# Performance work log

Hardware: AMD Instinct MI355X
Metric: run time of the kernel (lower is better)

The kernel has to match this reference:

```python
import jax, jax.numpy as jnp
import numpy as np

B, T, D, H, FF, L = 4, 2048, 512, 8, 2048, 4
IN_SIZE = 32
PAST, FUT = 128, 128
HD = D // H
EPS = 1e-5


def _layer_norm(x, g, b):
    m = jnp.mean(x, axis=-1, keepdims=True)
    v = jnp.mean((x - m) ** 2, axis=-1, keepdims=True)
    return (x - m) / jnp.sqrt(v + EPS) * g + b


def setup_inputs() -> dict:
    key = jax.random.key(0)
    ks = jax.random.split(key, 20)
    s = 0.02
    inp = {
        "beatmap_features": jax.random.normal(ks[0], (B, T, IN_SIZE), jnp.float32),
        "positions": jax.random.normal(ks[1], (B, T, 2), jnp.float32),
        "proj_w": jax.random.normal(ks[2], (D, IN_SIZE), jnp.float32) * s,
        "proj_b": jnp.zeros((D,), jnp.float32),
        "pos_enc": jax.random.normal(ks[3], (T, D), jnp.float32),
        # stacked per-layer params, leading dim L
        "qkv_w": jax.random.normal(ks[4], (L, 3 * D, D), jnp.float32) * s,
        "qkv_b": jnp.zeros((L, 3 * D), jnp.float32),
        "out_w": jax.random.normal(ks[5], (L, D, D), jnp.float32) * s,
        "out_b": jnp.zeros((L, D), jnp.float32),
        "ff1_w": jax.random.normal(ks[6], (L, FF, D), jnp.float32) * s,
        "ff1_b": jnp.zeros((L, FF), jnp.float32),
        "ff2_w": jax.random.normal(ks[7], (L, D, FF), jnp.float32) * s,
        "ff2_b": jnp.zeros((L, D), jnp.float32),
        "ln1_g": jnp.ones((L, D), jnp.float32),
        "ln1_b": jnp.zeros((L, D), jnp.float32),
        "ln2_g": jnp.ones((L, D), jnp.float32),
        "ln2_b": jnp.zeros((L, D), jnp.float32),
    }
    return inp


def reference(beatmap_features, positions, proj_w, proj_b, pos_enc,
              qkv_w, qkv_b, out_w, out_b, ff1_w, ff1_b, ff2_w, ff2_b,
              ln1_g, ln1_b, ln2_g, ln2_b):
    # positions only perturbed by noise during training; eval forward ignores it.
    x = beatmap_features @ proj_w.T + proj_b + pos_enc[None]  # [B,T,D]

    # banded local-window additive mask: allow j in [i-PAST, i+FUT]
    i = jnp.arange(T)[:, None]
    j = jnp.arange(T)[None, :]
    allow = (j >= i - PAST) & (j <= i + FUT)
    mask = jnp.where(allow, 0.0, -jnp.inf).astype(x.dtype)  # [T,T]

    scale = 1.0 / jnp.sqrt(jnp.asarray(HD, x.dtype))

    def enc_layer(x, p):
        qkvw, qkvb, ow, ob, f1w, f1b, f2w, f2b, g1, b1, g2, b2 = p
        qkv = x @ qkvw.T + qkvb                         # [B,T,3D]
        q, k, v = jnp.split(qkv, 3, axis=-1)
        q = q.reshape(B, T, H, HD).transpose(0, 2, 1, 3)  # [B,H,T,HD]
        k = k.reshape(B, T, H, HD).transpose(0, 2, 1, 3)
        v = v.reshape(B, T, H, HD).transpose(0, 2, 1, 3)
        scores = jnp.einsum('bhqd,bhkd->bhqk', q, k) * scale + mask
        attn = jax.nn.softmax(scores, axis=-1)
        o = jnp.einsum('bhqk,bhkd->bhqd', attn, v)
        o = o.transpose(0, 2, 1, 3).reshape(B, T, D) @ ow.T + ob
        x = _layer_norm(x + o, g1, b1)                  # post-norm (PyTorch default)
        h = jax.nn.relu(x @ f1w.T + f1b) @ f2w.T + f2b
        x = _layer_norm(x + h, g2, b2)
        return x, None

    params = (qkv_w, qkv_b, out_w, out_b, ff1_w, ff1_b, ff2_w, ff2_b,
              ln1_g, ln1_b, ln2_g, ln2_b)
    x, _ = jax.lax.scan(enc_layer, x, params)
    return x
```

## Files before the change

kernel.cpp:

```cpp
#include <hip/hip_runtime.h>
#include <hip/hip_bf16.h>

#define B_ 4
#define T_ 2048
#define D_ 512
#define H_ 8
#define FF_ 2048
#define L_ 4
#define NTOK 8192
#define EPS_ 1e-5f

typedef __hip_bfloat16 bf16;
typedef __attribute__((ext_vector_type(8))) short short8;
typedef __attribute__((ext_vector_type(4))) float floatx4;

__device__ __forceinline__ float bf2f(short s) {
    union { unsigned u; float f; } cv;
    cv.u = ((unsigned)(unsigned short)s) << 16;
    return cv.f;
}
__device__ __forceinline__ short f2bs(float f) {
    union { bf16 b; short s; } cv;
    cv.b = __float2bfloat16(f);
    return cv.s;
}

__global__ __launch_bounds__(256) void prep_kernel(
    const float* __restrict__ s0, const float* __restrict__ s1,
    const float* __restrict__ s2, const float* __restrict__ s3,
    bf16* __restrict__ dst, const float* __restrict__ pw, float* __restrict__ pwT)
{
    int bid = blockIdx.x;
    if (bid >= 12288) {
        int idx = (bid - 12288) * 256 + threadIdx.x;
        int d = idx >> 5, k = idx & 31;
        pwT[k * D_ + d] = pw[idx];
        return;
    }
    long i = (long)bid * 256 + threadIdx.x;
    const float* src; long off;
    if (i < 786432)       { src = s0; off = i; }
    else if (i < 1048576) { src = s1; off = i - 786432; }
    else if (i < 2097152) { src = s2; off = i - 1048576; }
    else                  { src = s3; off = i - 2097152; }
    float4 v = ((const float4*)src)[off];
    union { short s[4]; uint2 u; } pk;
    pk.s[0] = f2bs(v.x); pk.s[1] = f2bs(v.y);
    pk.s[2] = f2bs(v.z); pk.s[3] = f2bs(v.w);
    *(uint2*)((short*)dst + i * 4) = pk.u;
}

__global__ __launch_bounds__(256) void proj_kernel(
    const float* __restrict__ feat, const float* __restrict__ pwT,
    const float* __restrict__ pb, const float* __restrict__ pe,
    bf16* __restrict__ xb)
{
    __shared__ float fs[16][32];
    int tok0 = blockIdx.x * 16;
    int tid = threadIdx.x;
    {
        float2 v = ((const float2*)(feat + (size_t)tok0 * 32))[tid];
        fs[tid >> 4][(tid & 15) * 2]     = v.x;
        fs[tid >> 4][(tid & 15) * 2 + 1] = v.y;
    }
    int d0 = tid * 2;
    float w0[32], w1[32];
    #pragma unroll
    for (int k = 0; k < 32; k++) {
        float2 wv = *(const float2*)(pwT + k * D_ + d0);
        w0[k] = wv.x; w1[k] = wv.y;
    }
    float2 pbv = *(const float2*)(pb + d0);
    __syncthreads();
    #pragma unroll 4
    for (int tok = 0; tok < 16; tok++) {
        int t = (tok0 + tok) & (T_ - 1);
        float s0 = pbv.x, s1 = pbv.y;
        #pragma unroll
        for (int k = 0; k < 32; k++) {
            float f = fs[tok][k];
            s0 += f * w0[k]; s1 += f * w1[k];
        }
        float2 pev = *(const float2*)(pe + (size_t)t * D_ + d0);
        s0 += pev.x; s1 += pev.y;
        size_t o = (size_t)(tok0 + tok) * D_ + d0;
        union { struct { short a, b; } s; unsigned u; } pk;
        pk.s.a = f2bs(s0); pk.s.b = f2bs(s1);
        *(unsigned*)((short*)xb + o) = pk.u;
    }
}

template <int RELU>
__global__ __launch_bounds__(256) void gemm_bf16_kernel(
    const short* __restrict__ A, const short* __restrict__ W,
    const float* __restrict__ bias, bf16* __restrict__ Cb,
    int M, int N, int Kstride, int Kloc)
{
    __shared__ __align__(16) short lds[128 * 136];
    int bm = blockIdx.y * 128, bn = blockIdx.x * 128;
    int kbase = blockIdx.z * Kloc;
    int tid = threadIdx.x;
    int w = tid >> 6, lane = tid & 63;
    int wm = (w >> 1) * 64, wn = (w & 1) * 64;

    floatx4 acc[4][4];
    #pragma unroll
    for (int i = 0; i < 4; i++)
        #pragma unroll
        for (int j = 0; j < 4; j++)
            acc[i][j] = (floatx4){0.f, 0.f, 0.f, 0.f};

    int r0 = tid >> 2;
    int c0 = tid & 3;
    int slot = (c0 ^ ((r0 >> 1) & 3)) * 8;
    const short* Arow0 = A + (size_t)(bm + r0) * Kstride + kbase + c0 * 8;
    const short* Arow1 = A + (size_t)(bm + r0 + 64) * Kstride + kbase + c0 * 8;
    const short* Brow0 = W + (size_t)(bn + r0) * Kstride + kbase + c0 * 8;
    const short* Brow1 = W + (size_t)(bn + r0 + 64) * Kstride + kbase + c0 * 8;

    int lrow = lane & 15, lk = lane >> 4;

    short8 ea0, ea1, eb0, eb1;
    short8 oa0, oa1, ob0, ob1;
    ea0 = *(const short8*)(Arow0);       ea1 = *(const short8*)(Arow1);
    eb0 = *(const short8*)(Brow0);       eb1 = *(const short8*)(Brow1);
    oa0 = *(const short8*)(Arow0 + 32);  oa1 = *(const short8*)(Arow1 + 32);
    ob0 = *(const short8*)(Brow0 + 32);  ob1 = *(const short8*)(Brow1 + 32);

    int nIter = Kloc >> 5;
    for (int it = 0; it < nIter; it += 2) {
        #pragma unroll
        for (int half = 0; half < 2; half++) {
            short* As = lds + half * 8192;
            short* Bs = lds + half * 8192 + 4096;
            if (half == 0) {
                *(short8*)&As[r0 * 32 + slot] = ea0;
                *(short8*)&As[(r0 + 64) * 32 + slot] = ea1;
                *(short8*)&Bs[r0 * 32 + slot] = eb0;
                *(short8*)&Bs[(r0 + 64) * 32 + slot] = eb1;
            } else {
                *(short8*)&As[r0 * 32 + slot] = oa0;
                *(short8*)&As[(r0 + 64) * 32 + slot] = oa1;
                *(short8*)&Bs[r0 * 32 + slot] = ob0;
                *(short8*)&Bs[(r0 + 64) * 32 + slot] = ob1;
            }
            __syncthreads();
            int kn = (it + half + 2) * 32;
            if (kn < Kloc) {
                if (half == 0) {
                    ea0 = *(const short8*)(Arow0 + kn);
                    ea1 = *(const short8*)(Arow1 + kn);
                    eb0 = *(const short8*)(Brow0 + kn);
                    eb1 = *(const short8*)(Brow1 + kn);
                } else {
                    oa0 = *(const short8*)(Arow0 + kn);
                    oa1 = *(const short8*)(Arow1 + kn);
                    ob0 = *(const short8*)(Brow0 + kn);
                    ob1 = *(const short8*)(Brow1 + kn);
                }
            }
            short8 af[4], bfr[4];
            #pragma unroll
            for (int i = 0; i < 4; i++) {
                int rr = wm + i * 16 + lrow;
                af[i] = *(const short8*)&As[rr * 32 + ((lk ^ ((rr >> 1) & 3)) * 8)];
                int nn = wn + i * 16 + lrow;
                bfr[i] = *(const short8*)&Bs[nn * 32 + ((lk ^ ((nn >> 1) & 3)) * 8)];
            }
            #pragma unroll
            for (int i = 0; i < 4; i++)
                #pragma unroll
                for (int j = 0; j < 4; j++)
                    acc[i][j] = __builtin_amdgcn_mfma_f32_16x16x32_bf16(
                        af[i], bfr[j], acc[i][j], 0, 0, 0);
        }
    }

    __syncthreads();

    int cl = lane & 15, rq = lane >> 4;
    bool z0 = (blockIdx.z == 0);
    #pragma unroll
    for (int i = 0; i < 4; i++) {
        #pragma unroll
        for (int j = 0; j < 4; j++) {
            int col = wn + j * 16 + cl;
            float bv = z0 ? bias[bn + col] : 0.f;
            #pragma unroll
            for (int r = 0; r < 4; r++) {
                int row = wm + i * 16 + rq * 4 + r;
                float v = acc[i][j][r] + bv;
                if (RELU) v = fmaxf(v, 0.f);
                lds[row * 136 + col] = f2bs(v);
            }
        }
    }
    __syncthreads();

    bf16* Cz = Cb + (size_t)blockIdx.z * M * N;
    #pragma unroll
    for (int s = 0; s < 8; s++) {
        int idx = tid + 256 * s;
        int r = idx >> 4, c8 = (idx & 15) * 8;
        short8 v = *(const short8*)&lds[r * 136 + c8];
        *(short8*)((short*)Cz + (size_t)(bm + r) * N + bn + c8) = v;
    }
}

__global__ __launch_bounds__(256, 4) void attn_kernel(
    const short* __restrict__ qkv, bf16* __restrict__ out)
{
    __shared__ __align__(16) short Qs[64 * 72];
    __shared__ __align__(16) short Ks[64 * 72];
    __shared__ __align__(16) short Vt[64 * 72];
    __shared__ __align__(16) short Ps[64 * 72];

    int q0 = blockIdx.x * 64;
    int bh = blockIdx.y;
    int b = bh >> 3, h = bh & 7;
    int tid = threadIdx.x;
    int w = tid >> 6, lane = tid & 63;
    int col = lane & 15, quad = lane >> 4;

    const size_t base = (size_t)b * T_ * 3 * D_;
    const int roww = 3 * D_;
    const int qoff = h * 64, koff = D_ + h * 64, voff = 2 * D_ + h * 64;

    #pragma unroll
    for (int i = 0; i < 2; i++) {
        int idx = tid + 256 * i;
        int r = idx >> 3, c8 = (idx & 7) * 8;
        *(short8*)&Qs[r * 72 + c8] =
            *(const short8*)(qkv + base + (size_t)(q0 + r) * roww + qoff + c8);
    }

    float l_r[4] = {0.f, 0.f, 0.f, 0.f};
    floatx4 Oacc[4];
    #pragma unroll
    for (int j = 0; j < 4; j++) Oacc[j] = (floatx4){0.f, 0.f, 0.f, 0.f};

    int klo = max(0, q0 - 128), khi = min(T_, q0 + 192);
    const float scale = 0.125f;
    int qrow = q0 + w * 16 + quad * 4;

    for (int kt = klo; kt < khi; kt += 64) {
        __syncthreads();
        #pragma unroll
        for (int i = 0; i < 2; i++) {
            int idx = tid + 256 * i;
            int r = idx >> 3, c8 = (idx & 7) * 8;
            *(short8*)&Ks[r * 72 + c8] =
                *(const short8*)(qkv + base + (size_t)(kt + r) * roww + koff + c8);
            short8 v = *(const short8*)(qkv + base + (size_t)(kt + r) * roww + voff + c8);
            #pragma unroll
            for (int u = 0; u < 8; u++) Vt[(c8 + u) * 72 + r] = v[u];
        }
        __syncthreads();

        short8 aq0 = *(const short8*)&Qs[(w * 16 + col) * 72 + quad * 8];
        short8 aq1 = *(const short8*)&Qs[(w * 16 + col) * 72 + 32 + quad * 8];
        floatx4 Sacc[4];
        #pragma unroll
        for (int j = 0; j < 4; j++) {
            short8 bk0 = *(const short8*)&Ks[(j * 16 + col) * 72 + quad * 8];
            short8 bk1 = *(const short8*)&Ks[(j * 16 + col) * 72 + 32 + quad * 8];
            floatx4 s = (floatx4){0.f, 0.f, 0.f, 0.f};
            s = __builtin_amdgcn_mfma_f32_16x16x32_bf16(aq0, bk0, s, 0, 0, 0);
            s = __builtin_amdgcn_mfma_f32_16x16x32_bf16(aq1, bk1, s, 0, 0, 0);
            Sacc[j] = s;
        }

        float ps[4] = {0.f, 0.f, 0.f, 0.f};
        #pragma unroll
        for (int j = 0; j < 4; j++) {
            int key = kt + j * 16 + col;
            #pragma unroll
            for (int r = 0; r < 4; r++) {
                int dj = key - (qrow + r);
                float p = (dj < -128 || dj > 128) ? 0.f : __expf(Sacc[j][r] * scale);
                ps[r] += p;
                Ps[(w * 16 + quad * 4 + r) * 72 + j * 16 + col] = f2bs(p);
            }
        }
        #pragma unroll
        for (int off = 1; off < 16; off <<= 1)
            #pragma unroll
            for (int r = 0; r < 4; r++)
                ps[r] += __shfl_xor(ps[r], off);
        #pragma unroll
        for (int r = 0; r < 4; r++) l_r[r] += ps[r];

        __syncthreads();

        short8 ap0 = *(const short8*)&Ps[(w * 16 + col) * 72 + quad * 8];
        short8 ap1 = *(const short8*)&Ps[(w * 16 + col) * 72 + 32 + quad * 8];
        #pragma unroll
        for (int j = 0; j < 4; j++) {
            short8 bv0 = *(const short8*)&Vt[(j * 16 + col) * 72 + quad * 8];
            short8 bv1 = *(const short8*)&Vt[(j * 16 + col) * 72 + 32 + quad * 8];
            Oacc[j] = __builtin_amdgcn_mfma_f32_16x16x32_bf16(ap0, bv0, Oacc[j], 0, 0, 0);
            Oacc[j] = __builtin_amdgcn_mfma_f32_16x16x32_bf16(ap1, bv1, Oacc[j], 0, 0, 0);
        }
    }

    float invl[4];
    #pragma unroll
    for (int r = 0; r < 4; r++) invl[r] = 1.0f / l_r[r];
    #pragma unroll
    for (int j = 0; j < 4; j++)
        #pragma unroll
        for (int r = 0; r < 4; r++)
            out[(size_t)(b * T_ + qrow + r) * D_ + h * 64 + j * 16 + col] =
                __float2bfloat16(Oacc[j][r] * invl[r]);
}

__global__ __launch_bounds__(256) void add_ln_kernel(
    const short* __restrict__ xb, const short* __restrict__ d0,
    const short* __restrict__ d1,
    const float* __restrict__ g, const float* __restrict__ bta,
    bf16* __restrict__ outb, float* __restrict__ outf)
{
    int wave = threadIdx.x >> 6, lane = threadIdx.x & 63;
    int row = blockIdx.x * 4 + wave;
    int c0 = lane * 8;
    size_t o = (size_t)row * D_ + c0;
    short8 xv = *(const short8*)(xb + o);
    short8 a0 = *(const short8*)(d0 + o);
    short8 a1 = *(const short8*)(d1 + o);
    float v[8];
    float s = 0.f;
    #pragma unroll
    for (int i = 0; i < 8; i++) {
        v[i] = bf2f(xv[i]) + bf2f(a0[i]) + bf2f(a1[i]);
        s += v[i];
    }
    #pragma unroll
    for (int off = 32; off > 0; off >>= 1) s += __shfl_xor(s, off);
    float mean = s * (1.0f / D_);
    float var = 0.f;
    #pragma unroll
    for (int i = 0; i < 8; i++) { float c = v[i] - mean; var += c * c; }
    #pragma unroll
    for (int off = 32; off > 0; off >>= 1) var += __shfl_xor(var, off);
    float inv = rsqrtf(var * (1.0f / D_) + EPS_);
    float4 g0 = *(const float4*)(g + c0), g1 = *(const float4*)(g + c0 + 4);
    float4 b0 = *(const float4*)(bta + c0), b1 = *(const float4*)(bta + c0 + 4);
    float ov[8];
    ov[0] = (v[0] - mean) * inv * g0.x + b0.x;
    ov[1] = (v[1] - mean) * inv * g0.y + b0.y;
    ov[2] = (v[2] - mean) * inv * g0.z + b0.z;
    ov[3] = (v[3] - mean) * inv * g0.w + b0.w;
    ov[4] = (v[4] - mean) * inv * g1.x + b1.x;
    ov[5] = (v[5] - mean) * inv * g1.y + b1.y;
    ov[6] = (v[6] - mean) * inv * g1.z + b1.z;
    ov[7] = (v[7] - mean) * inv * g1.w + b1.w;
    short8 ob;
    #pragma unroll
    for (int i = 0; i < 8; i++) ob[i] = f2bs(ov[i]);
    *(short8*)((short*)outb + o) = ob;
    if (outf) {
        *(float4*)(outf + o) = make_float4(ov[0], ov[1], ov[2], ov[3]);
        *(float4*)(outf + o + 4) = make_float4(ov[4], ov[5], ov[6], ov[7]);
    }
}

extern "C" void kernel_launch(void* const* d_in, const int* in_sizes, int n_in,
                              void* d_out, int out_size, void* d_ws, size_t ws_size,
                              hipStream_t stream)
{
    const float* feat    = (const float*)d_in[0];
    const float* proj_w  = (const float*)d_in[2];
    const float* proj_b  = (const float*)d_in[3];
    const float* pos_enc = (const float*)d_in[4];
    const float* qkv_w   = (const float*)d_in[5];
    const float* qkv_b   = (const float*)d_in[6];
    const float* out_w   = (const float*)d_in[7];
    const float* out_b   = (const float*)d_in[8];
    const float* ff1_w   = (const float*)d_in[9];
    const float* ff1_b   = (const float*)d_in[10];
    const float* ff2_w   = (const float*)d_in[11];
    const float* ff2_b   = (const float*)d_in[12];
    const float* ln1_g   = (const float*)d_in[13];
    const float* ln1_b   = (const float*)d_in[14];
    const float* ln2_g   = (const float*)d_in[15];
    const float* ln2_b   = (const float*)d_in[16];

    char* p = (char*)d_ws;
    float* pwT  = (float*)p;  p += (size_t)32 * D_ * 4;
    bf16* xb    = (bf16*)p;   p += (size_t)NTOK * D_ * 2;
    bf16* dpar  = (bf16*)p;   p += (size_t)2 * NTOK * D_ * 2;
    bf16* qkvb  = (bf16*)p;   p += (size_t)NTOK * 3 * D_ * 2;
    bf16* hbuf  = (bf16*)p;   p += (size_t)NTOK * FF_ * 2;
    bf16* abuf  = (bf16*)p;   p += (size_t)NTOK * D_ * 2;
    bf16* wq    = (bf16*)p;   p += (size_t)L_ * 3 * D_ * D_ * 2;
    bf16* wo    = (bf16*)p;   p += (size_t)L_ * D_ * D_ * 2;
    bf16* w1    = (bf16*)p;   p += (size_t)L_ * FF_ * D_ * 2;
    bf16* w2    = (bf16*)p;   p += (size_t)L_ * D_ * FF_ * 2;
    float* outp = (float*)d_out;

    prep_kernel<<<12288 + 64, 256, 0, stream>>>(
        qkv_w, out_w, ff1_w, ff2_w, wq, proj_w, pwT);

    proj_kernel<<<NTOK / 16, 256, 0, stream>>>(feat, pwT, proj_b, pos_enc, xb);

    for (int l = 0; l < L_; l++) {
        gemm_bf16_kernel<0><<<dim3(3 * D_ / 128, NTOK / 128, 1), 256, 0, stream>>>(
            (const short*)xb, (const short*)(wq + (size_t)l * 3 * D_ * D_),
            qkv_b + (size_t)l * 3 * D_, qkvb, NTOK, 3 * D_, D_, D_);
        attn_kernel<<<dim3(T_ / 64, B_ * H_), 256, 0, stream>>>((const short*)qkvb, abuf);
        gemm_bf16_kernel<0><<<dim3(D_ / 128, NTOK / 128, 2), 256, 0, stream>>>(
            (const short*)abuf, (const short*)(wo + (size_t)l * D_ * D_),
            out_b + (size_t)l * D_, dpar, NTOK, D_, D_, D_ / 2);
        add_ln_kernel<<<NTOK / 4, 256, 0, stream>>>(
            (const short*)xb, (const short*)dpar, (const short*)(dpar + (size_t)NTOK * D_),
            ln1_g + (size_t)l * D_, ln1_b + (size_t)l * D_, xb, nullptr);
        gemm_bf16_kernel<1><<<dim3(FF_ / 128, NTOK / 128, 1), 256, 0, stream>>>(
            (const short*)xb, (const short*)(w1 + (size_t)l * FF_ * D_),
            ff1_b + (size_t)l * FF_, hbuf, NTOK, FF_, D_, D_);
        gemm_bf16_kernel<0><<<dim3(D_ / 128, NTOK / 128, 2), 256, 0, stream>>>(
            (const short*)hbuf, (const short*)(w2 + (size_t)l * D_ * FF_),
            ff2_b + (size_t)l * D_, dpar, NTOK, D_, FF_, FF_ / 2);
        float* dst = (l == L_ - 1) ? outp : nullptr;
        add_ln_kernel<<<NTOK / 4, 256, 0, stream>>>(
            (const short*)xb, (const short*)dpar, (const short*)(dpar + (size_t)NTOK * D_),
            ln2_g + (size_t)l * D_, ln2_b + (size_t)l * D_, xb, dst);
    }
}
```

Measured before the change: 660.0 us.

## Swizzle block IDs across XCDs and register-prefetch next K/V tile in attention

Adds an XCD-aware block-index swizzle to the GEMM and attention kernels so that neighbouring tiles, which share operands, land on the same XCD and its L2. In the attention kernel, the next K/V tile is loaded from global memory into registers while the current tile is being computed, hiding global load latency behind the MFMA work. This raises register pressure in a kernel launched with occupancy bound 4. The swizzle assumes the total block count is divisible by 8.

```diff
diff --git a/kernel.cpp b/kernel.cpp
--- a/kernel.cpp
+++ b/kernel.cpp
@@ -23,6 +23,10 @@
     union { bf16 b; short s; } cv;
     cv.b = __float2bfloat16(f);
     return cv.s;
+}
+
+__device__ __forceinline__ int xcd_swizzle(int id, int tot) {
+    return (id & 7) * (tot >> 3) + (id >> 3);
 }
 
 __global__ __launch_bounds__(256) void prep_kernel(
@@ -97,7 +101,10 @@
     int M, int N, int Kstride, int Kloc)
 {
     __shared__ __align__(16) short lds[128 * 136];
-    int bm = blockIdx.y * 128, bn = blockIdx.x * 128;
+    int nx = gridDim.x;
+    int id = blockIdx.y * nx + blockIdx.x;
+    int lid = xcd_swizzle(id, nx * gridDim.y);
+    int bm = (lid / nx) * 128, bn = (lid % nx) * 128;
     int kbase = blockIdx.z * Kloc;
     int tid = threadIdx.x;
     int w = tid >> 6, lane = tid & 63;
@@ -215,8 +222,10 @@
     __shared__ __align__(16) short Vt[64 * 72];
     __shared__ __align__(16) short Ps[64 * 72];
 
-    int q0 = blockIdx.x * 64;
-    int bh = blockIdx.y;
+    int id = blockIdx.y * 32 + blockIdx.x;
+    int lid = xcd_swizzle(id, 32 * B_ * H_);
+    int q0 = (lid % 32) * 64;
+    int bh = lid / 32;
     int b = bh >> 3, h = bh & 7;
     int tid = threadIdx.x;
     int w = tid >> 6, lane = tid & 63;
@@ -225,6 +234,9 @@
     const size_t base = (size_t)b * T_ * 3 * D_;
     const int roww = 3 * D_;
     const int qoff = h * 64, koff = D_ + h * 64, voff = 2 * D_ + h * 64;
+
+    int r_s = tid >> 3, c8_s = (tid & 7) * 8;
+    int r_s2 = r_s + 32;
 
     #pragma unroll
     for (int i = 0; i < 2; i++) {
@@ -243,17 +255,26 @@
     const float scale = 0.125f;
     int qrow = q0 + w * 16 + quad * 4;
 
+    short8 kreg0, kreg1, vreg0, vreg1;
+    kreg0 = *(const short8*)(qkv + base + (size_t)(klo + r_s) * roww + koff + c8_s);
+    kreg1 = *(const short8*)(qkv + base + (size_t)(klo + r_s2) * roww + koff + c8_s);
+    vreg0 = *(const short8*)(qkv + base + (size_t)(klo + r_s) * roww + voff + c8_s);
+    vreg1 = *(const short8*)(qkv + base + (size_t)(klo + r_s2) * roww + voff + c8_s);
+
     for (int kt = klo; kt < khi; kt += 64) {
         __syncthreads();
-        #pragma unroll
-        for (int i = 0; i < 2; i++) {
-            int idx = tid + 256 * i;
-            int r = idx >> 3, c8 = (idx & 7) * 8;
-            *(short8*)&Ks[r * 72 + c8] =
-                *(const short8*)(qkv + base + (size_t)(kt + r) * roww + koff + c8);
-            short8 v = *(const short8*)(qkv + base + (size_t)(kt + r) * roww + voff + c8);
-            #pragma unroll
-            for (int u = 0; u < 8; u++) Vt[(c8 + u) * 72 + r] = v[u];
+        *(short8*)&Ks[r_s * 72 + c8_s] = kreg0;
+        *(short8*)&Ks[r_s2 * 72 + c8_s] = kreg1;
+        #pragma unroll
+        for (int u = 0; u < 8; u++) Vt[(c8_s + u) * 72 + r_s] = vreg0[u];
+        #pragma unroll
+        for (int u = 0; u < 8; u++) Vt[(c8_s + u) * 72 + r_s2] = vreg1[u];
+        int ktn = kt + 64;
+        if (ktn < khi) {
+            kreg0 = *(const short8*)(qkv + base + (size_t)(ktn + r_s) * roww + koff + c8_s);
+            kreg1 = *(const short8*)(qkv + base + (size_t)(ktn + r_s2) * roww + koff + c8_s);
+            vreg0 = *(const short8*)(qkv + base + (size_t)(ktn + r_s) * roww + voff + c8_s);
+            vreg1 = *(const short8*)(qkv + base + (size_t)(ktn + r_s2) * roww + voff + c8_s);
         }
         __syncthreads();
 
```

Measured after the change: 617.8 us. 1.07x faster.
